# Optimization experiments

Measured on AMD Instinct MI355X. Metric: run time of the kernel, lower is better.

## Reference

```python
import jax, jax.numpy as jnp
import numpy as np

B, H, W = 2, 64, 64
D_MODEL, D_STATE, D_CONV, EXPAND = 192, 16, 3, 2
D_INNER = EXPAND * D_MODEL
DT_RANK = -(-D_MODEL // 16)  # ceil(d_model/16) = 12
L = H * W


def setup_inputs() -> dict:
    key = jax.random.key(0)
    ks = jax.random.split(key, 10)
    # dt bias init as in mamba: inverse-softplus of loguniform dt in [1e-3, 1e-1]
    dt = jnp.exp(jax.random.uniform(ks[9], (D_INNER,)) * (np.log(0.1) - np.log(0.001)) + np.log(0.001))
    dt = jnp.clip(dt, 1e-4, None)
    dt_proj_b = dt + jnp.log(-jnp.expm1(-dt))
    std = DT_RANK ** -0.5
    return {
        "x": jax.random.normal(ks[0], (B, H, W, D_MODEL), jnp.float32),
        "prompt": jax.random.normal(ks[1], (B, H, W, D_MODEL), jnp.float32),
        "in_proj_w": jax.random.normal(ks[2], (2 * D_INNER, D_MODEL), jnp.float32) * (D_MODEL ** -0.5),
        "conv_w": jax.random.normal(ks[3], (D_INNER, 1, D_CONV, D_CONV), jnp.float32) * (1.0 / 3.0),
        "conv_b": jax.random.normal(ks[4], (D_INNER,), jnp.float32) * 0.01,
        "x_proj_w": jax.random.normal(ks[5], (DT_RANK + 2 * D_STATE, D_INNER), jnp.float32) * (D_INNER ** -0.5),
        "dt_proj_w": jax.random.uniform(ks[6], (D_INNER, DT_RANK), jnp.float32, -std, std),
        "dt_proj_b": dt_proj_b,
        "A_log": jnp.log(jnp.tile(jnp.arange(1, D_STATE + 1, dtype=jnp.float32), (D_INNER, 1))),
        "Dp": jnp.ones((D_INNER,), jnp.float32),
        "prompt_proj_w": jax.random.normal(ks[7], (D_STATE, D_MODEL), jnp.float32) * (D_MODEL ** -0.5),
        "ln_g": jnp.ones((D_INNER,), jnp.float32),
        "ln_b": jnp.zeros((D_INNER,), jnp.float32),
        "out_proj_w": jax.random.normal(ks[8], (D_MODEL, D_INNER), jnp.float32) * (D_INNER ** -0.5),
    }


def selective_scan(u, delta, A, Bm, Cm, Dp, delta_bias):
    # u, delta: (B, d, L); A: (d, n); Bm, Cm: (B, n, L)
    delta = jax.nn.softplus(delta + delta_bias[None, :, None])
    dA = jnp.exp(jnp.einsum('bdl,dn->lbdn', delta, A))          # (L,B,d,n)
    dBu = jnp.einsum('bdl,bnl->lbdn', delta * u, Bm)            # (L,B,d,n)
    Ct = jnp.transpose(Cm, (2, 0, 1))                           # (L,B,n)
    h0 = jnp.zeros((u.shape[0], u.shape[1], A.shape[1]), u.dtype)

    def step(h, inp):
        dA_t, dBu_t, C_t = inp
        h = dA_t * h + dBu_t
        return h, jnp.einsum('bdn,bn->bd', h, C_t)

    _, ys = jax.lax.scan(step, h0, (dA, dBu, Ct))               # ys: (L,B,d)
    return jnp.transpose(ys, (1, 2, 0)) + Dp[None, :, None] * u  # (B,d,L)


def reference(x, prompt, in_proj_w, conv_w, conv_b, x_proj_w, dt_proj_w, dt_proj_b,
              A_log, Dp, prompt_proj_w, ln_g, ln_b, out_proj_w):
    b, h, w, _ = x.shape
    l = h * w
    xz = x @ in_proj_w.T                                        # (B,H,W,2*d_inner)
    xi, z = jnp.split(xz, 2, axis=-1)
    xc = jnp.transpose(xi, (0, 3, 1, 2))                        # NCHW
    xc = jax.lax.conv_general_dilated(
        xc, conv_w, (1, 1), 'SAME', feature_group_count=D_INNER,
        dimension_numbers=('NCHW', 'OIHW', 'NCHW')) + conv_b[None, :, None, None]
    xc = jax.nn.silu(xc)
    x_seq = jnp.transpose(xc.reshape(b, D_INNER, l), (0, 2, 1))  # (B,L,d)
    x_dbl = x_seq @ x_proj_w.T
    dt_low, B_ssm, C_ssm = jnp.split(x_dbl, [DT_RANK, DT_RANK + D_STATE], axis=-1)
    # NOTE: source applies dt_proj (with bias) AND passes delta_bias to the scan,
    # so the bias is added twice; reproduced faithfully.
    dt = jnp.transpose(dt_low @ dt_proj_w.T + dt_proj_b, (0, 2, 1))   # (B,d,L)
    B_ssm = jnp.transpose(B_ssm, (0, 2, 1))                          # (B,n,L)
    C_ssm = jnp.transpose(C_ssm, (0, 2, 1))                          # (B,n,L)
    prompt_c = jnp.transpose(prompt.reshape(b, l, -1) @ prompt_proj_w.T, (0, 2, 1))
    C_ssm = C_ssm + prompt_c
    A = -jnp.exp(A_log)
    u = jnp.transpose(x_seq, (0, 2, 1))                              # (B,d,L)
    y = selective_scan(u, dt, A, B_ssm, C_ssm, Dp, dt_proj_b)
    y = jnp.transpose(y, (0, 2, 1))                                  # (B,L,d)
    mu = y.mean(-1, keepdims=True)
    var = ((y - mu) ** 2).mean(-1, keepdims=True)
    y = (y - mu) / jnp.sqrt(var + 1e-5) * ln_g + ln_b
    y = y.reshape(b, h, w, D_INNER) * jax.nn.silu(z)
    return y @ out_proj_w.T
```

## Files before the change

kernel.cpp:

```cpp
#include <hip/hip_runtime.h>
#include <hip/hip_bf16.h>
#include <math.h>

#define BB 2
#define HH 64
#define WW 64
#define DM 192
#define DI 384
#define NS 16
#define RK 12
#define LL (HH*WW)
#define ML (BB*LL)
#define NC 256
#define CL 16

typedef __attribute__((ext_vector_type(8))) short short8v;
typedef __attribute__((ext_vector_type(4))) float f32x4;

__device__ __forceinline__ ushort f2bf(float f) {
  unsigned u = __float_as_uint(f);
  u += 0x7fffu + ((u >> 16) & 1u);
  return (ushort)(u >> 16);
}
__device__ __forceinline__ float bf2f(ushort h) {
  return __uint_as_float(((unsigned)h) << 16);
}
__device__ __forceinline__ void split2(float f, ushort& h, ushort& l) {
  h = f2bf(f);
  l = f2bf(f - bf2f(h));
}
__device__ __forceinline__ float softplus_fast(float x) {
  float e = __expf(-fabsf(x));
  return fmaxf(x, 0.f) + __logf(1.f + e);
}

__global__ __launch_bounds__(256) void prep(
    const float* __restrict__ w1, const float* __restrict__ w2,
    const float* __restrict__ wx, const float* __restrict__ x,
    const float* __restrict__ conv_w,
    ushort* __restrict__ w1h, ushort* __restrict__ w1l,
    ushort* __restrict__ w2h, ushort* __restrict__ w2l,
    ushort* __restrict__ wxh, ushort* __restrict__ wxl,
    ushort* __restrict__ xh,  ushort* __restrict__ xl,
    float* __restrict__ conv_wt) {
  const int Q1 = 768 * DM / 4;
  const int Q2 = DM * DI / 4;
  const int Q3 = 64 * DI / 4;
  const int Q4 = ML * DM / 4;
  const int QT = Q1 + Q2 + Q3 + Q4;
  int i = blockIdx.x * 256 + threadIdx.x;
  if (i < QT) {
    const float* src; ushort* dh; ushort* dl; int j;
    if (i < Q1)                { src = w1; dh = w1h; dl = w1l; j = i; }
    else if (i < Q1 + Q2)      { src = w2; dh = w2h; dl = w2l; j = i - Q1; }
    else if (i < Q1 + Q2 + Q3) { src = wx; dh = wxh; dl = wxl; j = i - Q1 - Q2; }
    else                       { src = x;  dh = xh;  dl = xl;  j = i - Q1 - Q2 - Q3; }
    float4 v;
    if (dh == wxh && j * 4 >= 44 * DI) v = make_float4(0.f, 0.f, 0.f, 0.f);
    else v = *reinterpret_cast<const float4*>(&src[(size_t)j * 4]);
    ushort4 h, l;
    split2(v.x, h.x, l.x); split2(v.y, h.y, l.y);
    split2(v.z, h.z, l.z); split2(v.w, h.w, l.w);
    *reinterpret_cast<ushort4*>(&dh[(size_t)j * 4]) = h;
    *reinterpret_cast<ushort4*>(&dl[(size_t)j * 4]) = l;
  } else if (i < QT + DI * 9) {
    int ct = i - QT;
    int k = ct % 9, d = ct / 9;
    conv_wt[k * DI + d] = conv_w[ct];
  }
}

template<int BM, int BN, int MR, int NR>
__global__ __launch_bounds__(256) void gemm_sp(
    const ushort* __restrict__ Ah, const ushort* __restrict__ Al,
    const ushort* __restrict__ Wh, const ushort* __restrict__ Wl,
    float* __restrict__ C, int M, int N, int K) {
  constexpr int RS = 40;
  __shared__ __align__(16) ushort sAh[BM * RS];
  __shared__ __align__(16) ushort sAl[BM * RS];
  __shared__ __align__(16) ushort sBh[BN * RS];
  __shared__ __align__(16) ushort sBl[BN * RS];
  const int tid = threadIdx.x;
  const int lane = tid & 63, wid = tid >> 6;
  const int wm = (wid >> 1) * (MR * 16);
  const int wn = (wid & 1) * (NR * 16);
  const int bm = blockIdx.y * BM;
  const int bn = blockIdx.x * BN;
  const int r16 = lane & 15;
  const int kb8 = (lane >> 4) * 8;

  f32x4 acc[MR][NR];
  #pragma unroll
  for (int m = 0; m < MR; ++m)
    #pragma unroll
    for (int n = 0; n < NR; ++n)
      acc[m][n] = (f32x4){0.f, 0.f, 0.f, 0.f};

  for (int k0 = 0; k0 < K; k0 += 32) {
    __syncthreads();
    for (int i = tid; i < BM * 4; i += 256) {
      int row = i >> 2, kc = (i & 3) << 3;
      *reinterpret_cast<short8v*>(&sAh[row * RS + kc]) =
          *reinterpret_cast<const short8v*>(&Ah[(size_t)(bm + row) * K + k0 + kc]);
      *reinterpret_cast<short8v*>(&sAl[row * RS + kc]) =
          *reinterpret_cast<const short8v*>(&Al[(size_t)(bm + row) * K + k0 + kc]);
    }
    for (int i = tid; i < BN * 4; i += 256) {
      int row = i >> 2, kc = (i & 3) << 3;
      *reinterpret_cast<short8v*>(&sBh[row * RS + kc]) =
          *reinterpret_cast<const short8v*>(&Wh[(size_t)(bn + row) * K + k0 + kc]);
      *reinterpret_cast<short8v*>(&sBl[row * RS + kc]) =
          *reinterpret_cast<const short8v*>(&Wl[(size_t)(bn + row) * K + k0 + kc]);
    }
    __syncthreads();

    short8v ah[MR], al[MR], bh[NR], bl[NR];
    #pragma unroll
    for (int m = 0; m < MR; ++m) {
      int off = (wm + m * 16 + r16) * RS + kb8;
      ah[m] = *reinterpret_cast<const short8v*>(&sAh[off]);
      al[m] = *reinterpret_cast<const short8v*>(&sAl[off]);
    }
    #pragma unroll
    for (int n = 0; n < NR; ++n) {
      int off = (wn + n * 16 + r16) * RS + kb8;
      bh[n] = *reinterpret_cast<const short8v*>(&sBh[off]);
      bl[n] = *reinterpret_cast<const short8v*>(&sBl[off]);
    }
    #pragma unroll
    for (int m = 0; m < MR; ++m)
      #pragma unroll
      for (int n = 0; n < NR; ++n)
        acc[m][n] = __builtin_amdgcn_mfma_f32_16x16x32_bf16(ah[m], bh[n], acc[m][n], 0, 0, 0);
    #pragma unroll
    for (int m = 0; m < MR; ++m)
      #pragma unroll
      for (int n = 0; n < NR; ++n)
        acc[m][n] = __builtin_amdgcn_mfma_f32_16x16x32_bf16(ah[m], bl[n], acc[m][n], 0, 0, 0);
    #pragma unroll
    for (int m = 0; m < MR; ++m)
      #pragma unroll
      for (int n = 0; n < NR; ++n)
        acc[m][n] = __builtin_amdgcn_mfma_f32_16x16x32_bf16(al[m], bh[n], acc[m][n], 0, 0, 0);
  }

  const int cr = (lane >> 4) * 4;
  #pragma unroll
  for (int m = 0; m < MR; ++m)
    #pragma unroll
    for (int n = 0; n < NR; ++n) {
      int row = bm + wm + m * 16 + cr;
      int col = bn + wn + n * 16 + r16;
      #pragma unroll
      for (int r = 0; r < 4; ++r)
        C[(size_t)(row + r) * N + col] = acc[m][n][r];
    }
}

__global__ __launch_bounds__(256) void conv_silu(const float* __restrict__ xz,
                                                 const float* __restrict__ conv_wt,
                                                 const float* __restrict__ conv_b,
                                                 float* __restrict__ x_seq,
                                                 ushort* __restrict__ xsh,
                                                 ushort* __restrict__ xsl) {
  int t = blockIdx.x * 256 + threadIdx.x;
  int d4 = (t % (DI / 4)) * 4;
  int l  = (t / (DI / 4)) % LL;
  int b  = t / ((DI / 4) * LL);
  int h = l >> 6, w = l & 63;
  float4 acc = *reinterpret_cast<const float4*>(&conv_b[d4]);
  #pragma unroll
  for (int kh = 0; kh < 3; ++kh) {
    int hh = h + kh - 1;
    if (hh < 0 || hh >= HH) continue;
    #pragma unroll
    for (int kw = 0; kw < 3; ++kw) {
      int ww2 = w + kw - 1;
      if (ww2 < 0 || ww2 >= WW) continue;
      float4 v = *reinterpret_cast<const float4*>(
          &xz[((size_t)(b * LL + hh * WW + ww2)) * 768 + d4]);
      float4 wv = *reinterpret_cast<const float4*>(&conv_wt[(kh * 3 + kw) * DI + d4]);
      acc.x = fmaf(v.x, wv.x, acc.x); acc.y = fmaf(v.y, wv.y, acc.y);
      acc.z = fmaf(v.z, wv.z, acc.z); acc.w = fmaf(v.w, wv.w, acc.w);
    }
  }
  float4 sv;
  sv.x = acc.x / (1.f + __expf(-acc.x));
  sv.y = acc.y / (1.f + __expf(-acc.y));
  sv.z = acc.z / (1.f + __expf(-acc.z));
  sv.w = acc.w / (1.f + __expf(-acc.w));
  size_t o = (size_t)t * 4;
  *reinterpret_cast<float4*>(&x_seq[o]) = sv;
  ushort4 hh4, ll4;
  split2(sv.x, hh4.x, ll4.x); split2(sv.y, hh4.y, ll4.y);
  split2(sv.z, hh4.z, ll4.z); split2(sv.w, hh4.w, ll4.w);
  *reinterpret_cast<ushort4*>(&xsh[o]) = hh4;
  *reinterpret_cast<ushort4*>(&xsl[o]) = ll4;
}

__global__ __launch_bounds__(DI) void mid_scan(
    const float* __restrict__ xdbl,
    const float* __restrict__ prompt,
    const float* __restrict__ xseq,
    const float* __restrict__ dt_proj_w,
    const float* __restrict__ dt_proj_b,
    const float* __restrict__ prompt_proj_w,
    const float* __restrict__ A_log,
    float* __restrict__ Bv, float* __restrict__ Cv,
    float* __restrict__ Pb, float* __restrict__ Qb) {
  const int d = threadIdx.x;
  const int c = blockIdx.x & (NC - 1);
  const int b = blockIdx.x >> 8;
  __shared__ __align__(16) float xd[CL][48];
  __shared__ __align__(16) float pr[CL][DM + 4];
  __shared__ __align__(16) float pw[NS][DM + 4];
  __shared__ __align__(16) float sB[CL][NS];
  const size_t row0 = (size_t)(b * LL + c * CL);

  for (int i = d; i < CL * 12; i += DI) {
    int r = i / 12, c4 = (i % 12) * 4;
    *reinterpret_cast<float4*>(&xd[r][c4]) =
        *reinterpret_cast<const float4*>(&xdbl[(row0 + r) * 64 + c4]);
  }
  for (int i = d; i < CL * 48; i += DI) {
    int r = i / 48, c4 = (i % 48) * 4;
    *reinterpret_cast<float4*>(&pr[r][c4]) =
        *reinterpret_cast<const float4*>(&prompt[(row0 + r) * DM + c4]);
  }
  for (int i = d; i < NS * 48; i += DI) {
    int r = i / 48, c4 = (i % 48) * 4;
    *reinterpret_cast<float4*>(&pw[r][c4]) =
        *reinterpret_cast<const float4*>(&prompt_proj_w[r * DM + c4]);
  }

  float sdtv[RK];
  #pragma unroll
  for (int j = 0; j < RK; j += 4) {
    float4 v = *reinterpret_cast<const float4*>(&dt_proj_w[(size_t)d * RK + j]);
    sdtv[j] = v.x; sdtv[j+1] = v.y; sdtv[j+2] = v.z; sdtv[j+3] = v.w;
  }
  const float db2 = 2.0f * dt_proj_b[d];
  float an[NS];
  #pragma unroll
  for (int n = 0; n < NS; n += 4) {
    float4 av = *reinterpret_cast<const float4*>(&A_log[d * NS + n]);
    an[n+0] = -__expf(av.x); an[n+1] = -__expf(av.y);
    an[n+2] = -__expf(av.z); an[n+3] = -__expf(av.w);
  }
  const size_t rowbase = row0 * DI + d;
  float xu[CL];
  #pragma unroll
  for (int s = 0; s < CL; ++s) xu[s] = xseq[rowbase + (size_t)s * DI];
  __syncthreads();

  float dlt[CL];
  float sum_de = 0.f;
  #pragma unroll
  for (int r = 0; r < CL; ++r) {
    float acc = db2;
    #pragma unroll
    for (int j = 0; j < RK; ++j) acc = fmaf(xd[r][j], sdtv[j], acc);
    dlt[r] = softplus_fast(acc);
    sum_de += dlt[r];
  }

  if (d < 256) {
    int r = d >> 4, n = d & 15;
    float bval = xd[r][12 + n];
    Bv[(row0 + r) * NS + n] = bval;
    sB[r][n] = bval;
    float acc = xd[r][28 + n];
    for (int c4 = 0; c4 < DM; c4 += 4) {
      float4 pv = *reinterpret_cast<const float4*>(&pr[r][c4]);
      float4 wv = *reinterpret_cast<const float4*>(&pw[n][c4]);
      acc = fmaf(pv.x, wv.x, acc); acc = fmaf(pv.y, wv.y, acc);
      acc = fmaf(pv.z, wv.z, acc); acc = fmaf(pv.w, wv.w, acc);
    }
    Cv[(row0 + r) * NS + n] = acc;
  }
  __syncthreads();

  float h[NS];
  #pragma unroll
  for (int n = 0; n < NS; ++n) h[n] = 0.f;
  #pragma unroll
  for (int s = 0; s < CL; ++s) {
    float de = dlt[s];
    float du = de * xu[s];
    float4 b0 = *reinterpret_cast<const float4*>(&sB[s][0]);
    float4 b1 = *reinterpret_cast<const float4*>(&sB[s][4]);
    float4 b2 = *reinterpret_cast<const float4*>(&sB[s][8]);
    float4 b3 = *reinterpret_cast<const float4*>(&sB[s][12]);
    float bb[NS] = {b0.x,b0.y,b0.z,b0.w, b1.x,b1.y,b1.z,b1.w,
                    b2.x,b2.y,b2.z,b2.w, b3.x,b3.y,b3.z,b3.w};
    #pragma unroll
    for (int n = 0; n < NS; ++n) {
      float e = __expf(de * an[n]);
      h[n] = fmaf(e, h[n], du * bb[n]);
    }
  }
  const size_t base = ((size_t)(b * NC + c) * DI + d) * NS;
  #pragma unroll
  for (int n = 0; n < NS; n += 4) {
    float4 pv = make_float4(__expf(sum_de * an[n]),   __expf(sum_de * an[n+1]),
                            __expf(sum_de * an[n+2]), __expf(sum_de * an[n+3]));
    *reinterpret_cast<float4*>(&Pb[base + n]) = pv;
    *reinterpret_cast<float4*>(&Qb[base + n]) = make_float4(h[n], h[n+1], h[n+2], h[n+3]);
  }
}

__global__ __launch_bounds__(256) void scan_combine(const float* __restrict__ Pb,
                                                    const float* __restrict__ Qb,
                                                    float* __restrict__ Hout) {
  const int tid = threadIdx.x;
  const int dnl = tid & 15;
  const int seg = tid >> 4;
  const int rec = blockIdx.x * 16 + dnl;
  const int b = rec / (DI * NS);
  const int dn = rec % (DI * NS);
  const size_t S = DI * NS;
  const size_t base = (size_t)b * NC * S + dn;

  float p[16], q[16];
  #pragma unroll
  for (int i = 0; i < 16; ++i) {
    p[i] = Pb[base + (size_t)(seg * 16 + i) * S];
    q[i] = Qb[base + (size_t)(seg * 16 + i) * S];
  }
  float Pa = 1.f, Qa = 0.f;
  #pragma unroll
  for (int i = 0; i < 16; ++i) { Qa = fmaf(p[i], Qa, q[i]); Pa *= p[i]; }

  __shared__ float sP[16][17], sQ[16][17], sH[16][17];
  sP[dnl][seg] = Pa; sQ[dnl][seg] = Qa;
  __syncthreads();
  if (tid < 16) {
    float hh = 0.f;
    #pragma unroll
    for (int s2 = 0; s2 < 16; ++s2) {
      sH[tid][s2] = hh;
      hh = fmaf(sP[tid][s2], hh, sQ[tid][s2]);
    }
  }
  __syncthreads();
  float h = sH[dnl][seg];
  #pragma unroll
  for (int i = 0; i < 16; ++i) {
    Hout[base + (size_t)(seg * 16 + i) * S] = h;
    h = fmaf(p[i], h, q[i]);
  }
}

__global__ __launch_bounds__(DI) void scan_pass2_ln(
    const float* __restrict__ xdbl, const float* __restrict__ x_seq,
    const float* __restrict__ Bv, const float* __restrict__ Cv,
    const float* __restrict__ dt_proj_w, const float* __restrict__ dt_proj_b,
    const float* __restrict__ A_log, const float* __restrict__ Dp,
    const float* __restrict__ hin, const float* __restrict__ xz,
    const float* __restrict__ ln_g, const float* __restrict__ ln_b,
    ushort* __restrict__ ygh, ushort* __restrict__ ygl) {
  const int d = threadIdx.x;
  const int c = blockIdx.x & (NC - 1);
  const int b = blockIdx.x >> 8;
  __shared__ __align__(16) float xd[CL][12];
  __shared__ float sB[CL][NS], sC[CL][NS];
  __shared__ float sY[CL][DI + 1];
  const size_t row0 = (size_t)(b * LL + c * CL);
  for (int idx = threadIdx.x; idx < CL * NS; idx += DI) {
    size_t g = (size_t)(b * LL + c * CL) * NS + idx;
    sB[idx >> 4][idx & 15] = Bv[g];
    sC[idx >> 4][idx & 15] = Cv[g];
  }
  for (int i = d; i < CL * 3; i += DI) {
    int r = i / 3, c4 = (i % 3) * 4;
    *reinterpret_cast<float4*>(&xd[r][c4]) =
        *reinterpret_cast<const float4*>(&xdbl[(row0 + r) * 64 + c4]);
  }
  const size_t rowbase = row0 * DI + d;
  float xu[CL];
  #pragma unroll
  for (int s = 0; s < CL; ++s) xu[s] = x_seq[rowbase + (size_t)s * DI];

  float sdtv[RK];
  #pragma unroll
  for (int j = 0; j < RK; j += 4) {
    float4 v = *reinterpret_cast<const float4*>(&dt_proj_w[(size_t)d * RK + j]);
    sdtv[j] = v.x; sdtv[j+1] = v.y; sdtv[j+2] = v.z; sdtv[j+3] = v.w;
  }
  const float db2 = 2.0f * dt_proj_b[d];
  float an[NS], h[NS];
  const size_t hbase = ((size_t)(b * NC + c) * DI + d) * NS;
  #pragma unroll
  for (int n = 0; n < NS; n += 4) {
    float4 hv = *reinterpret_cast<const float4*>(&hin[hbase + n]);
    h[n] = hv.x; h[n+1] = hv.y; h[n+2] = hv.z; h[n+3] = hv.w;
  }
  #pragma unroll
  for (int n = 0; n < NS; n += 4) {
    float4 av = *reinterpret_cast<const float4*>(&A_log[d * NS + n]);
    an[n+0] = -__expf(av.x); an[n+1] = -__expf(av.y);
    an[n+2] = -__expf(av.z); an[n+3] = -__expf(av.w);
  }
  const float Dd = Dp[d];
  __syncthreads();

  #pragma unroll
  for (int s = 0; s < CL; ++s) {
    float dacc = db2;
    #pragma unroll
    for (int j = 0; j < RK; ++j) dacc = fmaf(xd[s][j], sdtv[j], dacc);
    float de = softplus_fast(dacc);
    float u  = xu[s];
    float du = de * u;
    float acc = Dd * u;
    float4 b0 = *reinterpret_cast<const float4*>(&sB[s][0]);
    float4 b1 = *reinterpret_cast<const float4*>(&sB[s][4]);
    float4 b2 = *reinterpret_cast<const float4*>(&sB[s][8]);
    float4 b3 = *reinterpret_cast<const float4*>(&sB[s][12]);
    float bb[NS] = {b0.x,b0.y,b0.z,b0.w, b1.x,b1.y,b1.z,b1.w,
                    b2.x,b2.y,b2.z,b2.w, b3.x,b3.y,b3.z,b3.w};
    float4 c0 = *reinterpret_cast<const float4*>(&sC[s][0]);
    float4 c1 = *reinterpret_cast<const float4*>(&sC[s][4]);
    float4 c2 = *reinterpret_cast<const float4*>(&sC[s][8]);
    float4 c3 = *reinterpret_cast<const float4*>(&sC[s][12]);
    float cc[NS] = {c0.x,c0.y,c0.z,c0.w, c1.x,c1.y,c1.z,c1.w,
                    c2.x,c2.y,c2.z,c2.w, c3.x,c3.y,c3.z,c3.w};
    #pragma unroll
    for (int n = 0; n < NS; ++n) {
      float e = __expf(de * an[n]);
      h[n] = fmaf(e, h[n], du * bb[n]);
      acc = fmaf(h[n], cc[n], acc);
    }
    sY[s][d] = acc;
  }
  __syncthreads();

  const int wv = d >> 6, lane = d & 63;
  float lg[6], lb[6];
  #pragma unroll
  for (int k = 0; k < 6; ++k) { lg[k] = ln_g[lane + k * 64]; lb[k] = ln_b[lane + k * 64]; }
  for (int r = wv; r < CL; r += 6) {
    const size_t row = row0 + r;
    float v[6];
    float sum = 0.f, sq = 0.f;
    #pragma unroll
    for (int k = 0; k < 6; ++k) {
      v[k] = sY[r][lane + k * 64];
      sum += v[k];
      sq = fmaf(v[k], v[k], sq);
    }
    #pragma unroll
    for (int off = 32; off >= 1; off >>= 1) {
      sum += __shfl_xor(sum, off, 64);
      sq  += __shfl_xor(sq,  off, 64);
    }
    const float mu = sum * (1.f / DI);
    const float var = sq * (1.f / DI) - mu * mu;
    const float rstd = rsqrtf(var + 1e-5f);
    #pragma unroll
    for (int k = 0; k < 6; ++k) {
      int dd = lane + k * 64;
      float t = (v[k] - mu) * rstd * lg[k] + lb[k];
      float z = xz[row * 768 + DI + dd];
      float outv = t * (z / (1.f + __expf(-z)));
      ushort hh16, ll16;
      split2(outv, hh16, ll16);
      ygh[row * DI + dd] = hh16;
      ygl[row * DI + dd] = ll16;
    }
  }
}

extern "C" void kernel_launch(void* const* d_in, const int* in_sizes, int n_in,
                              void* d_out, int out_size, void* d_ws, size_t ws_size,
                              hipStream_t stream) {
  const float* x             = (const float*)d_in[0];
  const float* prompt        = (const float*)d_in[1];
  const float* in_proj_w     = (const float*)d_in[2];
  const float* conv_w        = (const float*)d_in[3];
  const float* conv_b        = (const float*)d_in[4];
  const float* x_proj_w      = (const float*)d_in[5];
  const float* dt_proj_w     = (const float*)d_in[6];
  const float* dt_proj_b     = (const float*)d_in[7];
  const float* A_log         = (const float*)d_in[8];
  const float* Dp            = (const float*)d_in[9];
  const float* prompt_proj_w = (const float*)d_in[10];
  const float* ln_g          = (const float*)d_in[11];
  const float* ln_b          = (const float*)d_in[12];
  const float* out_proj_w    = (const float*)d_in[13];
  float* out = (float*)d_out;

  char* p = (char*)d_ws;
  auto alloc = [&](size_t bytes) { char* r = p; p += (bytes + 255) & ~(size_t)255; return r; };
  float*  xz    = (float*)alloc((size_t)ML * 768 * 4);
  float*  xseq  = (float*)alloc((size_t)ML * DI * 4);
  float*  xdbl  = (float*)alloc((size_t)ML * 64 * 4);
  float*  bv    = (float*)alloc((size_t)ML * NS * 4);
  float*  cv    = (float*)alloc((size_t)ML * NS * 4);
  float*  pb    = (float*)alloc((size_t)BB * NC * DI * NS * 4);
  float*  qb    = (float*)alloc((size_t)BB * NC * DI * NS * 4);
  float*  hin   = (float*)alloc((size_t)BB * NC * DI * NS * 4);
  ushort* w1h   = (ushort*)alloc((size_t)768 * DM * 2);
  ushort* w1l   = (ushort*)alloc((size_t)768 * DM * 2);
  ushort* w2h   = (ushort*)alloc((size_t)DM * DI * 2);
  ushort* w2l   = (ushort*)alloc((size_t)DM * DI * 2);
  ushort* wxh   = (ushort*)alloc((size_t)64 * DI * 2);
  ushort* wxl   = (ushort*)alloc((size_t)64 * DI * 2);
  ushort* xh    = (ushort*)alloc((size_t)ML * DM * 2);
  ushort* xl    = (ushort*)alloc((size_t)ML * DM * 2);
  ushort* xsh   = (ushort*)alloc((size_t)ML * DI * 2);
  ushort* xsl   = (ushort*)alloc((size_t)ML * DI * 2);
  ushort* ygh   = (ushort*)alloc((size_t)ML * DI * 2);
  ushort* ygl   = (ushort*)alloc((size_t)ML * DI * 2);
  float*  cwt   = (float*)alloc((size_t)9 * DI * 4);

  prep<<<1790, 256, 0, stream>>>(in_proj_w, out_proj_w, x_proj_w, x, conv_w,
                                 w1h, w1l, w2h, w2l, wxh, wxl, xh, xl, cwt);
  gemm_sp<64, 96, 2, 3><<<dim3(8, 128), 256, 0, stream>>>(xh, xl, w1h, w1l, xz, ML, 768, DM);
  conv_silu<<<(ML * DI / 4) / 256, 256, 0, stream>>>(xz, cwt, conv_b, xseq, xsh, xsl);
  gemm_sp<32, 64, 1, 2><<<dim3(1, 256), 256, 0, stream>>>(xsh, xsl, wxh, wxl, xdbl, ML, 64, DI);
  mid_scan<<<BB * NC, DI, 0, stream>>>(xdbl, prompt, xseq, dt_proj_w, dt_proj_b,
                                       prompt_proj_w, A_log, bv, cv, pb, qb);
  scan_combine<<<(BB * DI * NS) / 16, 256, 0, stream>>>(pb, qb, hin);
  scan_pass2_ln<<<BB * NC, DI, 0, stream>>>(xdbl, xseq, bv, cv, dt_proj_w, dt_proj_b,
                                            A_log, Dp, hin, xz, ln_g, ln_b, ygh, ygl);
  gemm_sp<32, 64, 1, 2><<<dim3(3, 256), 256, 0, stream>>>(ygh, ygl, w2h, w2l, out, ML, DM, DI);
}
```

Baseline: 124.9 us.

## Fuse x_proj GEMM into mid-scan kernel using in-block MFMA

Removes the separate x_proj GEMM launch and computes the 16x64 x_dbl tile for each chunk inside the scan kernel, using split-bf16 MFMA on 4 of its 6 waves. Only the dt_low slice is written back to a smaller xdt buffer for the second scan pass, which cuts one launch and the full x_dbl round trip. In exchange, each of the 512 blocks reloads the whole 64x384 weight matrix and runs 12 sync-separated K steps, and two waves sit idle during the GEMM.

```diff
diff --git a/kernel.cpp b/kernel.cpp
--- a/kernel.cpp
+++ b/kernel.cpp
@@ -198,41 +198,45 @@
   *reinterpret_cast<ushort4*>(&xsl[o]) = ll4;
 }
 
-__global__ __launch_bounds__(DI) void mid_scan(
-    const float* __restrict__ xdbl,
+__global__ __launch_bounds__(DI) void xdbl_scan(
+    const ushort* __restrict__ xsh, const ushort* __restrict__ xsl,
+    const ushort* __restrict__ wxh, const ushort* __restrict__ wxl,
     const float* __restrict__ prompt,
     const float* __restrict__ xseq,
     const float* __restrict__ dt_proj_w,
     const float* __restrict__ dt_proj_b,
     const float* __restrict__ prompt_proj_w,
     const float* __restrict__ A_log,
+    float* __restrict__ xdt,
     float* __restrict__ Bv, float* __restrict__ Cv,
     float* __restrict__ Pb, float* __restrict__ Qb) {
-  const int d = threadIdx.x;
+  constexpr int RS = 40;
+  const int tid = threadIdx.x;
+  const int d = tid;
   const int c = blockIdx.x & (NC - 1);
   const int b = blockIdx.x >> 8;
-  __shared__ __align__(16) float xd[CL][48];
+  const int lane = tid & 63, wid = tid >> 6;
+  const int r16 = lane & 15;
+  const int kb8 = (lane >> 4) * 8;
+
+  __shared__ __align__(16) ushort sAh[16 * RS], sAl[16 * RS];
+  __shared__ __align__(16) ushort sBh[64 * RS], sBl[64 * RS];
+  __shared__ __align__(16) float xd[CL][64];
   __shared__ __align__(16) float pr[CL][DM + 4];
   __shared__ __align__(16) float pw[NS][DM + 4];
   __shared__ __align__(16) float sB[CL][NS];
   const size_t row0 = (size_t)(b * LL + c * CL);
 
-  for (int i = d; i < CL * 12; i += DI) {
-    int r = i / 12, c4 = (i % 12) * 4;
-    *reinterpret_cast<float4*>(&xd[r][c4]) =
-        *reinterpret_cast<const float4*>(&xdbl[(row0 + r) * 64 + c4]);
-  }
-  for (int i = d; i < CL * 48; i += DI) {
+  for (int i = tid; i < CL * 48; i += DI) {
     int r = i / 48, c4 = (i % 48) * 4;
     *reinterpret_cast<float4*>(&pr[r][c4]) =
         *reinterpret_cast<const float4*>(&prompt[(row0 + r) * DM + c4]);
   }
-  for (int i = d; i < NS * 48; i += DI) {
+  for (int i = tid; i < NS * 48; i += DI) {
     int r = i / 48, c4 = (i % 48) * 4;
     *reinterpret_cast<float4*>(&pw[r][c4]) =
         *reinterpret_cast<const float4*>(&prompt_proj_w[r * DM + c4]);
   }
-
   float sdtv[RK];
   #pragma unroll
   for (int j = 0; j < RK; j += 4) {
@@ -251,6 +255,44 @@
   float xu[CL];
   #pragma unroll
   for (int s = 0; s < CL; ++s) xu[s] = xseq[rowbase + (size_t)s * DI];
+
+  f32x4 acc4 = (f32x4){0.f, 0.f, 0.f, 0.f};
+  for (int k0 = 0; k0 < DI; k0 += 32) {
+    __syncthreads();
+    for (int i = tid; i < 64; i += DI) {
+      int row = i >> 2, kc = (i & 3) << 3;
+      *reinterpret_cast<short8v*>(&sAh[row * RS + kc]) =
+          *reinterpret_cast<const short8v*>(&xsh[(row0 + row) * DI + k0 + kc]);
+      *reinterpret_cast<short8v*>(&sAl[row * RS + kc]) =
+          *reinterpret_cast<const short8v*>(&xsl[(row0 + row) * DI + k0 + kc]);
+    }
+    for (int i = tid; i < 256; i += DI) {
+      int row = i >> 2, kc = (i & 3) << 3;
+      *reinterpret_cast<short8v*>(&sBh[row * RS + kc]) =
+          *reinterpret_cast<const short8v*>(&wxh[(size_t)row * DI + k0 + kc]);
+      *reinterpret_cast<short8v*>(&sBl[row * RS + kc]) =
+          *reinterpret_cast<const short8v*>(&wxl[(size_t)row * DI + k0 + kc]);
+    }
+    __syncthreads();
+    if (wid < 4) {
+      int aoff = r16 * RS + kb8;
+      int boff = (wid * 16 + r16) * RS + kb8;
+      short8v ah = *reinterpret_cast<const short8v*>(&sAh[aoff]);
+      short8v al = *reinterpret_cast<const short8v*>(&sAl[aoff]);
+      short8v bh = *reinterpret_cast<const short8v*>(&sBh[boff]);
+      short8v bl = *reinterpret_cast<const short8v*>(&sBl[boff]);
+      acc4 = __builtin_amdgcn_mfma_f32_16x16x32_bf16(ah, bh, acc4, 0, 0, 0);
+      acc4 = __builtin_amdgcn_mfma_f32_16x16x32_bf16(ah, bl, acc4, 0, 0, 0);
+      acc4 = __builtin_amdgcn_mfma_f32_16x16x32_bf16(al, bh, acc4, 0, 0, 0);
+    }
+  }
+  __syncthreads();
+  if (wid < 4) {
+    const int cr = (lane >> 4) * 4;
+    #pragma unroll
+    for (int r = 0; r < 4; ++r)
+      xd[cr + r][wid * 16 + r16] = acc4[r];
+  }
   __syncthreads();
 
   float dlt[CL];
@@ -263,7 +305,10 @@
     dlt[r] = softplus_fast(acc);
     sum_de += dlt[r];
   }
-
+  for (int i = tid; i < CL * RK; i += DI) {
+    int r = i / RK, j = i % RK;
+    xdt[(row0 + r) * RK + j] = xd[r][j];
+  }
   if (d < 256) {
     int r = d >> 4, n = d & 15;
     float bval = xd[r][12 + n];
@@ -352,7 +397,7 @@
 }
 
 __global__ __launch_bounds__(DI) void scan_pass2_ln(
-    const float* __restrict__ xdbl, const float* __restrict__ x_seq,
+    const float* __restrict__ xdt, const float* __restrict__ x_seq,
     const float* __restrict__ Bv, const float* __restrict__ Cv,
     const float* __restrict__ dt_proj_w, const float* __restrict__ dt_proj_b,
     const float* __restrict__ A_log, const float* __restrict__ Dp,
@@ -374,7 +419,7 @@
   for (int i = d; i < CL * 3; i += DI) {
     int r = i / 3, c4 = (i % 3) * 4;
     *reinterpret_cast<float4*>(&xd[r][c4]) =
-        *reinterpret_cast<const float4*>(&xdbl[(row0 + r) * 64 + c4]);
+        *reinterpret_cast<const float4*>(&xdt[(row0 + r) * RK + c4]);
   }
   const size_t rowbase = row0 * DI + d;
   float xu[CL];
@@ -494,7 +539,7 @@
   auto alloc = [&](size_t bytes) { char* r = p; p += (bytes + 255) & ~(size_t)255; return r; };
   float*  xz    = (float*)alloc((size_t)ML * 768 * 4);
   float*  xseq  = (float*)alloc((size_t)ML * DI * 4);
-  float*  xdbl  = (float*)alloc((size_t)ML * 64 * 4);
+  float*  xdt   = (float*)alloc((size_t)ML * RK * 4);
   float*  bv    = (float*)alloc((size_t)ML * NS * 4);
   float*  cv    = (float*)alloc((size_t)ML * NS * 4);
   float*  pb    = (float*)alloc((size_t)BB * NC * DI * NS * 4);
@@ -518,11 +563,11 @@
                                  w1h, w1l, w2h, w2l, wxh, wxl, xh, xl, cwt);
   gemm_sp<64, 96, 2, 3><<<dim3(8, 128), 256, 0, stream>>>(xh, xl, w1h, w1l, xz, ML, 768, DM);
   conv_silu<<<(ML * DI / 4) / 256, 256, 0, stream>>>(xz, cwt, conv_b, xseq, xsh, xsl);
-  gemm_sp<32, 64, 1, 2><<<dim3(1, 256), 256, 0, stream>>>(xsh, xsl, wxh, wxl, xdbl, ML, 64, DI);
-  mid_scan<<<BB * NC, DI, 0, stream>>>(xdbl, prompt, xseq, dt_proj_w, dt_proj_b,
-                                       prompt_proj_w, A_log, bv, cv, pb, qb);
+  xdbl_scan<<<BB * NC, DI, 0, stream>>>(xsh, xsl, wxh, wxl, prompt, xseq,
+                                        dt_proj_w, dt_proj_b, prompt_proj_w,
+                                        A_log, xdt, bv, cv, pb, qb);
   scan_combine<<<(BB * DI * NS) / 16, 256, 0, stream>>>(pb, qb, hin);
-  scan_pass2_ln<<<BB * NC, DI, 0, stream>>>(xdbl, xseq, bv, cv, dt_proj_w, dt_proj_b,
+  scan_pass2_ln<<<BB * NC, DI, 0, stream>>>(xdt, xseq, bv, cv, dt_proj_w, dt_proj_b,
                                             A_log, Dp, hin, xz, ln_g, ln_b, ygh, ygl);
   gemm_sp<32, 64, 1, 2><<<dim3(3, 256), 256, 0, stream>>>(ygh, ygl, w2h, w2l, out, ML, DM, DI);
 }
```

Result: slower. 128.3 us (+2.7%).
